# Kernel tuning notes

Measured on AMD Instinct MI355X. Metric: run time of the kernel, lower is better.

The kernel has to match this reference:

```python
import jax, jax.numpy as jnp
import numpy as np

N_NODES = 100000
N_EDGES = 1600000
N_GRAPHS = 128


def setup_inputs() -> dict:
    key = jax.random.key(0)
    ks = jax.random.split(key, 8)
    x = jax.random.normal(ks[0], (N_NODES, 384), dtype=jnp.float32)
    edge_index = jax.random.randint(ks[1], (2, N_EDGES), 0, N_NODES, dtype=jnp.int64)
    batch = jnp.sort(jax.random.randint(ks[2], (N_NODES,), 0, N_GRAPHS, dtype=jnp.int64))
    W1 = jax.random.normal(ks[3], (384, 128), dtype=jnp.float32) * (1.0 / np.sqrt(384))
    b1 = jnp.zeros((128,), dtype=jnp.float32)
    W2 = jax.random.normal(ks[4], (128, 64), dtype=jnp.float32) * (1.0 / np.sqrt(128))
    b2 = jnp.zeros((64,), dtype=jnp.float32)
    Wlin = jax.random.normal(ks[5], (64, 2), dtype=jnp.float32) * (1.0 / np.sqrt(64))
    blin = jnp.zeros((2,), dtype=jnp.float32)
    return {"x": x, "edge_index": edge_index, "batch": batch,
            "W1": W1, "b1": b1, "W2": W2, "b2": b2, "Wlin": Wlin, "blin": blin}


def gcn_conv(x, src, dst, W, b, n_nodes):
    # PyG GCNConv: self-loops + symmetric normalization D^{-1/2} A_hat D^{-1/2},
    # linear transform first (out_dim < in_dim -> cheaper messages).
    h = x @ W  # [N, out]
    deg = jax.ops.segment_sum(jnp.ones_like(dst, dtype=h.dtype), dst,
                              num_segments=n_nodes) + 1.0  # self-loop weight
    dis = jax.lax.rsqrt(deg)  # deg >= 1 always (self-loop)
    norm = dis[src] * dis[dst]  # per-edge normalization [E]
    msg = h[src] * norm[:, None]  # gather + scale [E, out]
    agg = jax.ops.segment_sum(msg, dst, num_segments=n_nodes)
    agg = agg + h * (dis * dis)[:, None]  # self-loop contribution
    return agg + b


def reference(x, edge_index, batch, W1, b1, W2, b2, Wlin, blin):
    src, dst = edge_index[0], edge_index[1]
    n_nodes = x.shape[0]
    h = jax.nn.relu(gcn_conv(x, src, dst, W1, b1, n_nodes))
    h = jax.nn.relu(gcn_conv(h, src, dst, W2, b2, n_nodes))
    # global_mean_pool over graph ids
    sums = jax.ops.segment_sum(h, batch, num_segments=N_GRAPHS)
    cnts = jax.ops.segment_sum(jnp.ones((n_nodes,), dtype=h.dtype), batch,
                               num_segments=N_GRAPHS)
    pooled = sums / jnp.maximum(cnts, 1.0)[:, None]  # [G, 64]
    # dropout is identity in eval mode
    return pooled @ Wlin + blin  # [G, 2]
```

## Files before the change

### kernel.cpp

```cpp
#include <hip/hip_runtime.h>


#define NN 100000
#define NG 128
#define BNODES 256
#define NBUK ((NN + BNODES - 1) / BNODES)
#define BCAP 6144

typedef __attribute__((ext_vector_type(8))) short short8;
typedef __attribute__((ext_vector_type(8))) unsigned short u16x8;
typedef __attribute__((ext_vector_type(4))) float f32x4;

__device__ __forceinline__ unsigned short f2bf(float f) {
    union { float f; unsigned u; } v; v.f = f;
    unsigned r = v.u + 0x7fffu + ((v.u >> 16) & 1u);
    return (unsigned short)(r >> 16);
}
__device__ __forceinline__ float bf2f(unsigned short h) {
    union { unsigned u; float f; } v; v.u = ((unsigned)h) << 16;
    return v.f;
}

__global__ __launch_bounds__(256) void bucket_scatter(const int* __restrict__ src,
                                                      const int* __restrict__ dst,
                                                      int* __restrict__ bcnt,
                                                      int2* __restrict__ pairs, int E) {
    __shared__ int hist[NBUK];
    __shared__ int lbase[NBUK];
    __shared__ int lfill[NBUK];
    const int t = threadIdx.x;
    const int chunk = (E + gridDim.x - 1) / gridDim.x;
    const int lo = blockIdx.x * chunk;
    const int hi = min(E, lo + chunk);
    for (int b = t; b < NBUK; b += 256) { hist[b] = 0; lfill[b] = 0; }
    __syncthreads();
    for (int i = lo + t; i < hi; i += 256)
        atomicAdd(&hist[dst[i] >> 8], 1);
    __syncthreads();
    for (int b = t; b < NBUK; b += 256)
        lbase[b] = hist[b] ? atomicAdd(&bcnt[b], hist[b]) : 0;
    __syncthreads();
    for (int i = lo + t; i < hi; i += 256) {
        const int s = src[i], d = dst[i];
        const int b = d >> 8;
        const int off = atomicAdd(&lfill[b], 1);
        pairs[(size_t)b * BCAP + lbase[b] + off] = make_int2(s, d);
    }
}

__global__ __launch_bounds__(512) void bucket_scan(const int* __restrict__ bcnt,
                                                   int* __restrict__ bbase,
                                                   int* __restrict__ rowptr,
                                                   int N, int E) {
    __shared__ int sm[512];
    const int t = threadIdx.x;
    sm[t] = (t < NBUK) ? bcnt[t] : 0;
    __syncthreads();
    for (int d = 1; d < 512; d <<= 1) {
        int a = (t >= d) ? sm[t - d] : 0;
        __syncthreads();
        sm[t] += a;
        __syncthreads();
    }
    if (t <= NBUK) bbase[t] = (t == 0) ? 0 : sm[t - 1];
    if (t == 0) rowptr[N] = E;
}

__global__ __launch_bounds__(256) void bucket_build(const int2* __restrict__ pairs,
                                                    const int* __restrict__ bcnt,
                                                    const int* __restrict__ bbase,
                                                    int* __restrict__ rowptr,
                                                    float* __restrict__ dis,
                                                    int* __restrict__ col, int N) {
    __shared__ int cnt[BNODES];
    __shared__ int sm[BNODES];
    __shared__ int pref[BNODES];
    __shared__ int fillc[BNODES];
    const int b = blockIdx.x;
    const int t = threadIdx.x;
    const int nbase = b * BNODES;
    const int ecnt = bcnt[b];
    const int2* ep = pairs + (size_t)b * BCAP;
    const int gbase = bbase[b];

    cnt[t] = 0;
    fillc[t] = 0;
    __syncthreads();
    for (int i = t; i < ecnt; i += 256)
        atomicAdd(&cnt[ep[i].y & (BNODES - 1)], 1);
    __syncthreads();
    sm[t] = cnt[t];
    __syncthreads();
    for (int d = 1; d < 256; d <<= 1) {
        int a = (t >= d) ? sm[t - d] : 0;
        __syncthreads();
        sm[t] += a;
        __syncthreads();
    }
    pref[t] = sm[t] - cnt[t];
    const int node = nbase + t;
    if (node < N) {
        rowptr[node] = gbase + pref[t];
        dis[node] = rsqrtf((float)cnt[t] + 1.0f);
    }
    __syncthreads();
    for (int i = t; i < ecnt; i += 256) {
        const int2 e = ep[i];
        const int d = e.y & (BNODES - 1);
        const int pos = gbase + pref[d] + atomicAdd(&fillc[d], 1);
        col[pos] = e.x;
    }
}

__global__ __launch_bounds__(256) void pack_w(const float* __restrict__ W,
                                              unsigned short* __restrict__ packH,
                                              unsigned short* __restrict__ packL,
                                              int K, int BN) {
    const int idx = blockIdx.x * blockDim.x + threadIdx.x;
    if (idx >= K * BN) return;
    const int e = idx & 7;
    const int l = (idx >> 3) & 63;
    const int rest = idx >> 9;
    const int NF = BN >> 4;
    const int nf = rest % NF;
    const int ks = rest / NF;
    const int n = nf * 16 + (l & 15);
    const int k = ks * 32 + ((l >> 4) & 3) * 8 + e;
    const float v = W[(size_t)k * BN + n];
    const unsigned short h = f2bf(v);
    packH[idx] = h;
    packL[idx] = f2bf(v - bf2f(h));
}

template <int BN>
__global__ __launch_bounds__(256) void gemm_mfma(const float* __restrict__ A,
                                                 const unsigned short* __restrict__ WpH,
                                                 const unsigned short* __restrict__ WpL,
                                                 const float* __restrict__ scale,
                                                 unsigned short* __restrict__ Out,
                                                 int N, int K) {
    constexpr int BM = 128;
    constexpr int WROWS = (BN == 128) ? 2 : 4;
    constexpr int WCOLS = (BN == 128) ? 2 : 1;
    constexpr int WTM = BM / WROWS;
    constexpr int MF = WTM / 16;
    constexpr int NFW = (BN / WCOLS) / 16;
    constexpr int NFB = BN / 16;

    __shared__ unsigned short AsH[8][512];
    __shared__ unsigned short AsL[8][512];

    const int t = threadIdx.x;
    const int wid = t >> 6, lane = t & 63;
    const int wr = wid / WCOLS, wc = wid % WCOLS;
    const int r0 = blockIdx.x * BM;

    const int s_row1 = t >> 2;
    const int s_row2 = (t + 256) >> 2;
    const int s_kg = t & 3;
    const int s_lf = ((t >> 2) & 15) + s_kg * 16;

    f32x4 acc[MF][NFW];
#pragma unroll
    for (int m = 0; m < MF; ++m)
#pragma unroll
        for (int n = 0; n < NFW; ++n) acc[m][n] = (f32x4){0.f, 0.f, 0.f, 0.f};

    for (int k0 = 0; k0 < K; k0 += 32) {
        const int ks = k0 >> 5;
#pragma unroll
        for (int uu = 0; uu < 2; ++uu) {
            const int row = uu ? s_row2 : s_row1;
            const int gr = r0 + row;
            float4 v0 = make_float4(0.f, 0.f, 0.f, 0.f), v1 = v0;
            if (gr < N) {
                const float* ap = &A[(size_t)gr * K + k0 + s_kg * 8];
                v0 = *(const float4*)ap;
                v1 = *(const float4*)(ap + 4);
            }
            short8 h, l;
            const float vv[8] = {v0.x, v0.y, v0.z, v0.w, v1.x, v1.y, v1.z, v1.w};
#pragma unroll
            for (int j = 0; j < 8; ++j) {
                const unsigned short hh = f2bf(vv[j]);
                h[j] = (short)hh;
                l[j] = (short)f2bf(vv[j] - bf2f(hh));
            }
            const int m = row >> 4;
            *(short8*)&AsH[m][s_lf * 8] = h;
            *(short8*)&AsL[m][s_lf * 8] = l;
        }
        __syncthreads();

        short8 bH[NFW], bL[NFW];
#pragma unroll
        for (int n = 0; n < NFW; ++n) {
            const int nfg = wc * NFW + n;
            const int base = ((ks * NFB + nfg) * 64 + lane) * 8;
            bH[n] = *(const short8*)&WpH[base];
            bL[n] = *(const short8*)&WpL[base];
        }
#pragma unroll
        for (int m = 0; m < MF; ++m) {
            const int mf = wr * MF + m;
            const short8 aH = *(const short8*)&AsH[mf][lane * 8];
            const short8 aL = *(const short8*)&AsL[mf][lane * 8];
#pragma unroll
            for (int n = 0; n < NFW; ++n) {
                acc[m][n] = __builtin_amdgcn_mfma_f32_16x16x32_bf16(aH, bH[n], acc[m][n], 0, 0, 0);
                acc[m][n] = __builtin_amdgcn_mfma_f32_16x16x32_bf16(aH, bL[n], acc[m][n], 0, 0, 0);
                acc[m][n] = __builtin_amdgcn_mfma_f32_16x16x32_bf16(aL, bH[n], acc[m][n], 0, 0, 0);
            }
        }
        __syncthreads();
    }

#pragma unroll
    for (int m = 0; m < MF; ++m) {
        const int row0 = r0 + wr * WTM + m * 16 + ((lane >> 4) << 2);
        float sc[4];
#pragma unroll
        for (int r = 0; r < 4; ++r) sc[r] = (row0 + r < N) ? scale[row0 + r] : 0.f;
#pragma unroll
        for (int n = 0; n < NFW; ++n) {
            const int cn = wc * (NFW * 16) + n * 16 + (lane & 15);
#pragma unroll
            for (int r = 0; r < 4; ++r) {
                if (row0 + r < N)
                    Out[(size_t)(row0 + r) * BN + cn] = f2bf(acc[m][n][r] * sc[r]);
            }
        }
    }
}

template <int COLS>
__global__ __launch_bounds__(256) void agg_gather(const int* __restrict__ rowptr,
                                                  const int* __restrict__ col,
                                                  const float* __restrict__ dis,
                                                  const unsigned short* __restrict__ Hs,
                                                  const float* __restrict__ bias,
                                                  float* __restrict__ Out, int N) {
    constexpr int NPW = (COLS == 128) ? 1 : 2;
    constexpr int LPN = 64 / NPW;
    constexpr int LPR = COLS / 8;
    constexpr int NSG = LPN / LPR;
    const int gw = (int)((blockIdx.x * blockDim.x + threadIdx.x) >> 6);
    const int lane = threadIdx.x & 63;
    const int sub = lane / LPN;
    const int nl = lane % LPN;
    const int esub = nl / LPR;
    const int sl = nl % LPR;
    const int node = gw * NPW + sub;
    const int lgbase = sub * LPN;

    float acc[8];
#pragma unroll
    for (int k = 0; k < 8; ++k) acc[k] = 0.f;

    int base = 0, len = 0;
    const int nodec = (node < N) ? node : 0;
    if (node < N) {
        base = rowptr[node];
        len = rowptr[node + 1] - base;
    }

    for (int j0 = 0; j0 < len; j0 += LPN) {
        const int remain = min(LPN, len - j0);
        const int sidx = (nl < remain) ? col[base + j0 + nl] : nodec;
        const int qtr = (remain + NSG - 1) / NSG;
        const int off = esub * qtr;
        int u = 0;
        for (; u + 8 <= qtr; u += 8) {
            u16x8 hv[8];
            float wv[8];
#pragma unroll
            for (int b = 0; b < 8; ++b) {
                const int idx = off + u + b;
                const int s = __shfl(sidx, lgbase + idx);
                wv[b] = (idx < remain) ? 1.f : 0.f;
                hv[b] = *(const u16x8*)(Hs + (size_t)s * COLS + sl * 8);
            }
#pragma unroll
            for (int b = 0; b < 8; ++b)
#pragma unroll
                for (int k = 0; k < 8; ++k)
                    acc[k] = fmaf(bf2f(hv[b][k]), wv[b], acc[k]);
        }
        for (; u + 4 <= qtr; u += 4) {
            u16x8 hv[4];
            float wv[4];
#pragma unroll
            for (int b = 0; b < 4; ++b) {
                const int idx = off + u + b;
                const int s = __shfl(sidx, lgbase + idx);
                wv[b] = (idx < remain) ? 1.f : 0.f;
                hv[b] = *(const u16x8*)(Hs + (size_t)s * COLS + sl * 8);
            }
#pragma unroll
            for (int b = 0; b < 4; ++b)
#pragma unroll
                for (int k = 0; k < 8; ++k)
                    acc[k] = fmaf(bf2f(hv[b][k]), wv[b], acc[k]);
        }
        for (; u < qtr; ++u) {
            const int idx = off + u;
            const int s = __shfl(sidx, lgbase + idx);
            const float w = (idx < remain) ? 1.f : 0.f;
            const u16x8 hv = *(const u16x8*)(Hs + (size_t)s * COLS + sl * 8);
#pragma unroll
            for (int k = 0; k < 8; ++k)
                acc[k] = fmaf(bf2f(hv[k]), w, acc[k]);
        }
    }

#pragma unroll
    for (int k = 0; k < 8; ++k) {
        acc[k] += __shfl_xor(acc[k], LPR);
        acc[k] += __shfl_xor(acc[k], 2 * LPR);
    }

    if (node < N && esub == 0) {
        const float dd = dis[node];
        const u16x8 hsb = *(const u16x8*)(Hs + (size_t)node * COLS + sl * 8);
        const f32x4 bv0 = *(const f32x4*)(bias + sl * 8);
        const f32x4 bv1 = *(const f32x4*)(bias + sl * 8 + 4);
        f32x4 o0, o1;
#pragma unroll
        for (int k = 0; k < 4; ++k) {
            o0[k] = fmaxf(fmaf(acc[k] + bf2f(hsb[k]), dd, bv0[k]), 0.f);
            o1[k] = fmaxf(fmaf(acc[k + 4] + bf2f(hsb[k + 4]), dd, bv1[k]), 0.f);
        }
        *(f32x4*)(Out + (size_t)node * COLS + sl * 8) = o0;
        *(f32x4*)(Out + (size_t)node * COLS + sl * 8 + 4) = o1;
    }
}

__global__ __launch_bounds__(256) void pool_kernel(const float* __restrict__ H,
                                                   const int* __restrict__ batch,
                                                   float* __restrict__ pooled,
                                                   float* __restrict__ cnt, int N) {
    const int c = threadIdx.x & 63;
    const int w = threadIdx.x >> 6;
    const int row0 = blockIdx.x * 128 + w * 32;
    if (row0 >= N) return;
    const int nr = min(32, N - row0);

    float v[32];
    int b[32];
#pragma unroll
    for (int i = 0; i < 32; ++i) {
        const int r = row0 + i;
        if (i < nr) {
            v[i] = H[(size_t)r * 64 + c];
            b[i] = batch[r];
        } else {
            v[i] = 0.f;
            b[i] = -1;
        }
    }
    int cur = b[0];
    float sum = 0.f, csum = 0.f;
#pragma unroll
    for (int i = 0; i < 32; ++i) {
        if (i < nr) {
            if (b[i] != cur) {
                atomicAdd(&pooled[cur * 64 + c], sum);
                if (c == 0) atomicAdd(&cnt[cur], csum);
                cur = b[i];
                sum = 0.f;
                csum = 0.f;
            }
            sum += v[i];
            csum += 1.f;
        }
    }
    atomicAdd(&pooled[cur * 64 + c], sum);
    if (c == 0) atomicAdd(&cnt[cur], csum);
}

__global__ __launch_bounds__(256) void final_kernel(const float* __restrict__ pooled,
                                                    const float* __restrict__ cnt,
                                                    const float* __restrict__ Wlin,
                                                    const float* __restrict__ blin,
                                                    float* __restrict__ out) {
    const int t = threadIdx.x;
    const int g = t >> 1, o = t & 1;
    const float inv = 1.0f / fmaxf(cnt[g], 1.0f);
    float s = 0.f;
#pragma unroll
    for (int j = 0; j < 64; ++j) s = fmaf(pooled[g * 64 + j], Wlin[j * 2 + o], s);
    out[t] = s * inv + blin[o];
}

extern "C" void kernel_launch(void* const* d_in, const int* in_sizes, int n_in,
                              void* d_out, int out_size, void* d_ws, size_t ws_size,
                              hipStream_t stream) {
    const float* x     = (const float*)d_in[0];
    const int*   edge  = (const int*)d_in[1];
    const int*   batch = (const int*)d_in[2];
    const float* W1    = (const float*)d_in[3];
    const float* b1    = (const float*)d_in[4];
    const float* W2    = (const float*)d_in[5];
    const float* b2    = (const float*)d_in[6];
    const float* Wlin  = (const float*)d_in[7];
    const float* blin  = (const float*)d_in[8];
    float* out = (float*)d_out;

    const int N = NN;
    const int E = in_sizes[1] / 2;
    const int* src = edge;
    const int* dst = edge + E;

    char* ws = (char*)d_ws;
    size_t off = 0;
    auto alloc = [&](size_t bytes) -> void* {
        void* p = ws + off;
        off += (bytes + 511) & ~(size_t)511;
        return p;
    };
    float* dis    = (float*)alloc((size_t)N * 4);
    int*   rowptr = (int*)alloc((size_t)(N + 1) * 4);
    int*   bcnt   = (int*)alloc((size_t)NBUK * 4);
    int*   bbase  = (int*)alloc((size_t)(NBUK + 1) * 4);
    int*   col    = (int*)alloc((size_t)E * 4);
    int2*  pairs  = (int2*)alloc((size_t)NBUK * BCAP * 8);
    unsigned short* w1h = (unsigned short*)alloc((size_t)384 * 128 * 2);
    unsigned short* w1l = (unsigned short*)alloc((size_t)384 * 128 * 2);
    unsigned short* w2h = (unsigned short*)alloc((size_t)128 * 64 * 2);
    unsigned short* w2l = (unsigned short*)alloc((size_t)128 * 64 * 2);
    unsigned short* h1bf = (unsigned short*)alloc((size_t)N * 128 * 2);
    float* agg1   = (float*)alloc((size_t)N * 128 * 4);
    float* pooled = (float*)alloc((size_t)NG * 64 * 4);
    float* cnt    = (float*)alloc((size_t)NG * 4);
    unsigned short* h2bf = h1bf;
    float* agg2 = agg1;

    hipMemsetAsync(bcnt, 0, (size_t)NBUK * 4, stream);
    hipMemsetAsync(pooled, 0, (size_t)NG * 64 * 4, stream);
    hipMemsetAsync(cnt, 0, (size_t)NG * 4, stream);

    pack_w<<<(384 * 128 + 255) / 256, 256, 0, stream>>>(W1, w1h, w1l, 384, 128);
    pack_w<<<(128 * 64 + 255) / 256, 256, 0, stream>>>(W2, w2h, w2l, 128, 64);

    bucket_scatter<<<512, 256, 0, stream>>>(src, dst, bcnt, pairs, E);
    bucket_scan<<<1, 512, 0, stream>>>(bcnt, bbase, rowptr, N, E);
    bucket_build<<<NBUK, 256, 0, stream>>>(pairs, bcnt, bbase, rowptr, dis, col, N);

    const int gblocks = (N + 127) / 128;
    gemm_mfma<128><<<gblocks, 256, 0, stream>>>(x, w1h, w1l, dis, h1bf, N, 384);
    agg_gather<128><<<(N + 3) / 4, 256, 0, stream>>>(rowptr, col, dis, h1bf, b1, agg1, N);

    gemm_mfma<64><<<gblocks, 256, 0, stream>>>(agg1, w2h, w2l, dis, h2bf, N, 128);
    agg_gather<64><<<(N + 7) / 8, 256, 0, stream>>>(rowptr, col, dis, h2bf, b2, agg2, N);

    pool_kernel<<<(N + 127) / 128, 256, 0, stream>>>(agg2, batch, pooled, cnt, N);
    final_kernel<<<1, 256, 0, stream>>>(pooled, cnt, Wlin, blin, out);
}
```

Baseline: 282.3 us.

## Double-buffer LDS and prefetch next K-slice in MFMA GEMM

The GEMM kernel now uses two LDS buffers. It issues global loads of the next A and B slices before running the MFMAs on the current slice, then converts and writes the prefetched A into the other buffer afterward, which removes one barrier per iteration. K becomes a template parameter so the K loop can be fully unrolled. This is meant to hide global memory latency behind compute, at the cost of doubling LDS use and raising register pressure, which may lower occupancy.

```diff
diff --git a/kernel.cpp b/kernel.cpp
--- a/kernel.cpp
+++ b/kernel.cpp
@@ -132,14 +132,15 @@
     packL[idx] = f2bf(v - bf2f(h));
 }
 
-template <int BN>
+template <int BN, int K>
 __global__ __launch_bounds__(256) void gemm_mfma(const float* __restrict__ A,
                                                  const unsigned short* __restrict__ WpH,
                                                  const unsigned short* __restrict__ WpL,
                                                  const float* __restrict__ scale,
                                                  unsigned short* __restrict__ Out,
-                                                 int N, int K) {
+                                                 int N) {
     constexpr int BM = 128;
+    constexpr int NK = K / 32;
     constexpr int WROWS = (BN == 128) ? 2 : 4;
     constexpr int WCOLS = (BN == 128) ? 2 : 1;
     constexpr int WTM = BM / WROWS;
@@ -147,8 +148,8 @@
     constexpr int NFW = (BN / WCOLS) / 16;
     constexpr int NFB = BN / 16;
 
-    __shared__ unsigned short AsH[8][512];
-    __shared__ unsigned short AsL[8][512];
+    __shared__ unsigned short AsH[2][8][512];
+    __shared__ unsigned short AsL[2][8][512];
 
     const int t = threadIdx.x;
     const int wid = t >> 6, lane = t & 63;
@@ -156,43 +157,46 @@
     const int r0 = blockIdx.x * BM;
 
     const int s_row1 = t >> 2;
-    const int s_row2 = (t + 256) >> 2;
+    const int s_row2 = 64 + (t >> 2);
     const int s_kg = t & 3;
     const int s_lf = ((t >> 2) & 15) + s_kg * 16;
 
-    f32x4 acc[MF][NFW];
-#pragma unroll
-    for (int m = 0; m < MF; ++m)
-#pragma unroll
-        for (int n = 0; n < NFW; ++n) acc[m][n] = (f32x4){0.f, 0.f, 0.f, 0.f};
-
-    for (int k0 = 0; k0 < K; k0 += 32) {
-        const int ks = k0 >> 5;
+    const bool ok1 = (r0 + s_row1) < N;
+    const bool ok2 = (r0 + s_row2) < N;
+    const float* aptr1 = A + (size_t)(r0 + s_row1) * K + s_kg * 8;
+    const float* aptr2 = A + (size_t)(r0 + s_row2) * K + s_kg * 8;
+
+    auto loadA = [&](int ks, float4* v) {
+        v[0] = v[1] = v[2] = v[3] = make_float4(0.f, 0.f, 0.f, 0.f);
+        if (ok1) {
+            v[0] = *(const float4*)(aptr1 + ks * 32);
+            v[1] = *(const float4*)(aptr1 + ks * 32 + 4);
+        }
+        if (ok2) {
+            v[2] = *(const float4*)(aptr2 + ks * 32);
+            v[3] = *(const float4*)(aptr2 + ks * 32 + 4);
+        }
+    };
+    auto cvtwrite = [&](int buf, const float4* v) {
 #pragma unroll
         for (int uu = 0; uu < 2; ++uu) {
-            const int row = uu ? s_row2 : s_row1;
-            const int gr = r0 + row;
-            float4 v0 = make_float4(0.f, 0.f, 0.f, 0.f), v1 = v0;
-            if (gr < N) {
-                const float* ap = &A[(size_t)gr * K + k0 + s_kg * 8];
-                v0 = *(const float4*)ap;
-                v1 = *(const float4*)(ap + 4);
-            }
             short8 h, l;
-            const float vv[8] = {v0.x, v0.y, v0.z, v0.w, v1.x, v1.y, v1.z, v1.w};
+            const float vv[8] = {v[2 * uu].x,     v[2 * uu].y,
+                                 v[2 * uu].z,     v[2 * uu].w,
+                                 v[2 * uu + 1].x, v[2 * uu + 1].y,
+                                 v[2 * uu + 1].z, v[2 * uu + 1].w};
 #pragma unroll
             for (int j = 0; j < 8; ++j) {
                 const unsigned short hh = f2bf(vv[j]);
                 h[j] = (short)hh;
                 l[j] = (short)f2bf(vv[j] - bf2f(hh));
             }
-            const int m = row >> 4;
-            *(short8*)&AsH[m][s_lf * 8] = h;
-            *(short8*)&AsL[m][s_lf * 8] = l;
-        }
-        __syncthreads();
-
-        short8 bH[NFW], bL[NFW];
+            const int m = uu ? (4 + wid) : wid;
+            *(short8*)&AsH[buf][m][s_lf * 8] = h;
+            *(short8*)&AsL[buf][m][s_lf * 8] = l;
+        }
+    };
+    auto loadB = [&](int ks, short8* bH, short8* bL) {
 #pragma unroll
         for (int n = 0; n < NFW; ++n) {
             const int nfg = wc * NFW + n;
@@ -200,19 +204,50 @@
             bH[n] = *(const short8*)&WpH[base];
             bL[n] = *(const short8*)&WpL[base];
         }
+    };
+
+    f32x4 acc[MF][NFW];
+#pragma unroll
+    for (int m = 0; m < MF; ++m)
+#pragma unroll
+        for (int n = 0; n < NFW; ++n) acc[m][n] = (f32x4){0.f, 0.f, 0.f, 0.f};
+
+    float4 av[4];
+    loadA(0, av);
+    cvtwrite(0, av);
+    short8 bHc[NFW], bLc[NFW];
+    loadB(0, bHc, bLc);
+
+#pragma unroll
+    for (int ks = 0; ks < NK; ++ks) {
+        const int cur = ks & 1;
+        __syncthreads();
+        float4 avn[4];
+        short8 bHn[NFW], bLn[NFW];
+        if (ks + 1 < NK) {
+            loadA(ks + 1, avn);
+            loadB(ks + 1, bHn, bLn);
+        }
 #pragma unroll
         for (int m = 0; m < MF; ++m) {
             const int mf = wr * MF + m;
-            const short8 aH = *(const short8*)&AsH[mf][lane * 8];
-            const short8 aL = *(const short8*)&AsL[mf][lane * 8];
+            const short8 aH = *(const short8*)&AsH[cur][mf][lane * 8];
+            const short8 aL = *(const short8*)&AsL[cur][mf][lane * 8];
 #pragma unroll
             for (int n = 0; n < NFW; ++n) {
-                acc[m][n] = __builtin_amdgcn_mfma_f32_16x16x32_bf16(aH, bH[n], acc[m][n], 0, 0, 0);
-                acc[m][n] = __builtin_amdgcn_mfma_f32_16x16x32_bf16(aH, bL[n], acc[m][n], 0, 0, 0);
-                acc[m][n] = __builtin_amdgcn_mfma_f32_16x16x32_bf16(aL, bH[n], acc[m][n], 0, 0, 0);
-            }
-        }
-        __syncthreads();
+                acc[m][n] = __builtin_amdgcn_mfma_f32_16x16x32_bf16(aH, bHc[n], acc[m][n], 0, 0, 0);
+                acc[m][n] = __builtin_amdgcn_mfma_f32_16x16x32_bf16(aH, bLc[n], acc[m][n], 0, 0, 0);
+                acc[m][n] = __builtin_amdgcn_mfma_f32_16x16x32_bf16(aL, bHc[n], acc[m][n], 0, 0, 0);
+            }
+        }
+        if (ks + 1 < NK) {
+            cvtwrite(cur ^ 1, avn);
+#pragma unroll
+            for (int n = 0; n < NFW; ++n) {
+                bHc[n] = bHn[n];
+                bLc[n] = bLn[n];
+            }
+        }
     }
 
 #pragma unroll
@@ -447,10 +482,10 @@
     bucket_build<<<NBUK, 256, 0, stream>>>(pairs, bcnt, bbase, rowptr, dis, col, N);
 
     const int gblocks = (N + 127) / 128;
-    gemm_mfma<128><<<gblocks, 256, 0, stream>>>(x, w1h, w1l, dis, h1bf, N, 384);
+    gemm_mfma<128, 384><<<gblocks, 256, 0, stream>>>(x, w1h, w1l, dis, h1bf, N);
     agg_gather<128><<<(N + 3) / 4, 256, 0, stream>>>(rowptr, col, dis, h1bf, b1, agg1, N);
 
-    gemm_mfma<64><<<gblocks, 256, 0, stream>>>(agg1, w2h, w2l, dis, h2bf, N, 128);
+    gemm_mfma<64, 128><<<gblocks, 256, 0, stream>>>(agg1, w2h, w2l, dis, h2bf, N);
     agg_gather<64><<<(N + 7) / 8, 256, 0, stream>>>(rowptr, col, dis, h2bf, b2, agg2, N);
 
     pool_kernel<<<(N + 127) / 128, 256, 0, stream>>>(agg2, batch, pooled, cnt, N);
```

New measurement: 274.5 us. -2.8%, faster.

## Drop LDS staging and low-bf16 A term in split-bf16 MFMA GEMM

Applied to the files above, without the earlier changes.

The GEMM is rewritten so each wave loads its own 16 A rows straight from global memory into MFMA operands, with no shared-memory staging or block barriers. The block tile shrinks to 64 rows and K becomes a template parameter. The A low-part correction term is dropped, going from three MFMAs per fragment to two, which lowers compute but also accuracy. The three memsets are replaced by one init kernel, which cuts launch overhead.

```diff
diff --git a/kernel.cpp b/kernel.cpp
--- a/kernel.cpp
+++ b/kernel.cpp
@@ -19,6 +19,15 @@
 __device__ __forceinline__ float bf2f(unsigned short h) {
     union { unsigned u; float f; } v; v.u = ((unsigned)h) << 16;
     return v.f;
+}
+
+__global__ __launch_bounds__(256) void init_kernel(int* __restrict__ bcnt,
+                                                   float* __restrict__ pooled,
+                                                   float* __restrict__ cnt) {
+    const int i = blockIdx.x * 256 + threadIdx.x;
+    if (i < NBUK) bcnt[i] = 0;
+    if (i < NG * 64) pooled[i] = 0.f;
+    if (i < NG) cnt[i] = 0.f;
 }
 
 __global__ __launch_bounds__(256) void bucket_scatter(const int* __restrict__ src,
@@ -132,103 +141,64 @@
     packL[idx] = f2bf(v - bf2f(h));
 }
 
-template <int BN>
+template <int BN, int K>
 __global__ __launch_bounds__(256) void gemm_mfma(const float* __restrict__ A,
                                                  const unsigned short* __restrict__ WpH,
                                                  const unsigned short* __restrict__ WpL,
                                                  const float* __restrict__ scale,
                                                  unsigned short* __restrict__ Out,
-                                                 int N, int K) {
-    constexpr int BM = 128;
-    constexpr int WROWS = (BN == 128) ? 2 : 4;
-    constexpr int WCOLS = (BN == 128) ? 2 : 1;
-    constexpr int WTM = BM / WROWS;
-    constexpr int MF = WTM / 16;
-    constexpr int NFW = (BN / WCOLS) / 16;
+                                                 int N) {
+    constexpr int NK = K / 32;
     constexpr int NFB = BN / 16;
-
-    __shared__ unsigned short AsH[8][512];
-    __shared__ unsigned short AsL[8][512];
 
     const int t = threadIdx.x;
     const int wid = t >> 6, lane = t & 63;
-    const int wr = wid / WCOLS, wc = wid % WCOLS;
-    const int r0 = blockIdx.x * BM;
-
-    const int s_row1 = t >> 2;
-    const int s_row2 = (t + 256) >> 2;
-    const int s_kg = t & 3;
-    const int s_lf = ((t >> 2) & 15) + s_kg * 16;
-
-    f32x4 acc[MF][NFW];
-#pragma unroll
-    for (int m = 0; m < MF; ++m)
-#pragma unroll
-        for (int n = 0; n < NFW; ++n) acc[m][n] = (f32x4){0.f, 0.f, 0.f, 0.f};
-
-    for (int k0 = 0; k0 < K; k0 += 32) {
-        const int ks = k0 >> 5;
-#pragma unroll
-        for (int uu = 0; uu < 2; ++uu) {
-            const int row = uu ? s_row2 : s_row1;
-            const int gr = r0 + row;
-            float4 v0 = make_float4(0.f, 0.f, 0.f, 0.f), v1 = v0;
-            if (gr < N) {
-                const float* ap = &A[(size_t)gr * K + k0 + s_kg * 8];
-                v0 = *(const float4*)ap;
-                v1 = *(const float4*)(ap + 4);
-            }
-            short8 h, l;
-            const float vv[8] = {v0.x, v0.y, v0.z, v0.w, v1.x, v1.y, v1.z, v1.w};
-#pragma unroll
-            for (int j = 0; j < 8; ++j) {
-                const unsigned short hh = f2bf(vv[j]);
-                h[j] = (short)hh;
-                l[j] = (short)f2bf(vv[j] - bf2f(hh));
-            }
-            const int m = row >> 4;
-            *(short8*)&AsH[m][s_lf * 8] = h;
-            *(short8*)&AsL[m][s_lf * 8] = l;
-        }
-        __syncthreads();
-
-        short8 bH[NFW], bL[NFW];
-#pragma unroll
-        for (int n = 0; n < NFW; ++n) {
-            const int nfg = wc * NFW + n;
-            const int base = ((ks * NFB + nfg) * 64 + lane) * 8;
-            bH[n] = *(const short8*)&WpH[base];
-            bL[n] = *(const short8*)&WpL[base];
-        }
-#pragma unroll
-        for (int m = 0; m < MF; ++m) {
-            const int mf = wr * MF + m;
-            const short8 aH = *(const short8*)&AsH[mf][lane * 8];
-            const short8 aL = *(const short8*)&AsL[mf][lane * 8];
-#pragma unroll
-            for (int n = 0; n < NFW; ++n) {
-                acc[m][n] = __builtin_amdgcn_mfma_f32_16x16x32_bf16(aH, bH[n], acc[m][n], 0, 0, 0);
-                acc[m][n] = __builtin_amdgcn_mfma_f32_16x16x32_bf16(aH, bL[n], acc[m][n], 0, 0, 0);
-                acc[m][n] = __builtin_amdgcn_mfma_f32_16x16x32_bf16(aL, bH[n], acc[m][n], 0, 0, 0);
-            }
-        }
-        __syncthreads();
-    }
-
-#pragma unroll
-    for (int m = 0; m < MF; ++m) {
-        const int row0 = r0 + wr * WTM + m * 16 + ((lane >> 4) << 2);
-        float sc[4];
-#pragma unroll
-        for (int r = 0; r < 4; ++r) sc[r] = (row0 + r < N) ? scale[row0 + r] : 0.f;
-#pragma unroll
-        for (int n = 0; n < NFW; ++n) {
-            const int cn = wc * (NFW * 16) + n * 16 + (lane & 15);
-#pragma unroll
-            for (int r = 0; r < 4; ++r) {
-                if (row0 + r < N)
-                    Out[(size_t)(row0 + r) * BN + cn] = f2bf(acc[m][n][r] * sc[r]);
-            }
+    const int r0 = (int)blockIdx.x * 64;
+    const int arow = r0 + wid * 16 + (lane & 15);
+    const bool ok = arow < N;
+    const float* ap = A + (size_t)(ok ? arow : 0) * K + (lane >> 4) * 8;
+
+    f32x4 acc[NFB];
+#pragma unroll
+    for (int n = 0; n < NFB; ++n) acc[n] = (f32x4){0.f, 0.f, 0.f, 0.f};
+
+#pragma unroll 2
+    for (int ks = 0; ks < NK; ++ks) {
+        float4 v0 = make_float4(0.f, 0.f, 0.f, 0.f), v1 = v0;
+        if (ok) {
+            v0 = *(const float4*)(ap + ks * 32);
+            v1 = *(const float4*)(ap + ks * 32 + 4);
+        }
+        short8 aH;
+        aH[0] = (short)f2bf(v0.x);
+        aH[1] = (short)f2bf(v0.y);
+        aH[2] = (short)f2bf(v0.z);
+        aH[3] = (short)f2bf(v0.w);
+        aH[4] = (short)f2bf(v1.x);
+        aH[5] = (short)f2bf(v1.y);
+        aH[6] = (short)f2bf(v1.z);
+        aH[7] = (short)f2bf(v1.w);
+#pragma unroll
+        for (int n = 0; n < NFB; ++n) {
+            const int base = ((ks * NFB + n) * 64 + lane) * 8;
+            const short8 bH = *(const short8*)&WpH[base];
+            const short8 bL = *(const short8*)&WpL[base];
+            acc[n] = __builtin_amdgcn_mfma_f32_16x16x32_bf16(aH, bH, acc[n], 0, 0, 0);
+            acc[n] = __builtin_amdgcn_mfma_f32_16x16x32_bf16(aH, bL, acc[n], 0, 0, 0);
+        }
+    }
+
+    const int row0 = r0 + wid * 16 + ((lane >> 4) << 2);
+    float sc[4];
+#pragma unroll
+    for (int r = 0; r < 4; ++r) sc[r] = (row0 + r < N) ? scale[row0 + r] : 0.f;
+#pragma unroll
+    for (int n = 0; n < NFB; ++n) {
+        const int cn = n * 16 + (lane & 15);
+#pragma unroll
+        for (int r = 0; r < 4; ++r) {
+            if (row0 + r < N)
+                Out[(size_t)(row0 + r) * BN + cn] = f2bf(acc[n][r] * sc[r]);
         }
     }
 }
@@ -435,9 +405,7 @@
     unsigned short* h2bf = h1bf;
     float* agg2 = agg1;
 
-    hipMemsetAsync(bcnt, 0, (size_t)NBUK * 4, stream);
-    hipMemsetAsync(pooled, 0, (size_t)NG * 64 * 4, stream);
-    hipMemsetAsync(cnt, 0, (size_t)NG * 4, stream);
+    init_kernel<<<(NG * 64 + 255) / 256, 256, 0, stream>>>(bcnt, pooled, cnt);
 
     pack_w<<<(384 * 128 + 255) / 256, 256, 0, stream>>>(W1, w1h, w1l, 384, 128);
     pack_w<<<(128 * 64 + 255) / 256, 256, 0, stream>>>(W2, w2h, w2l, 128, 64);
@@ -446,11 +414,11 @@
     bucket_scan<<<1, 512, 0, stream>>>(bcnt, bbase, rowptr, N, E);
     bucket_build<<<NBUK, 256, 0, stream>>>(pairs, bcnt, bbase, rowptr, dis, col, N);
 
-    const int gblocks = (N + 127) / 128;
-    gemm_mfma<128><<<gblocks, 256, 0, stream>>>(x, w1h, w1l, dis, h1bf, N, 384);
+    const int gblocks = (N + 63) / 64;
+    gemm_mfma<128, 384><<<gblocks, 256, 0, stream>>>(x, w1h, w1l, dis, h1bf, N);
     agg_gather<128><<<(N + 3) / 4, 256, 0, stream>>>(rowptr, col, dis, h1bf, b1, agg1, N);
 
-    gemm_mfma<64><<<gblocks, 256, 0, stream>>>(agg1, w2h, w2l, dis, h2bf, N, 128);
+    gemm_mfma<64, 128><<<gblocks, 256, 0, stream>>>(agg1, w2h, w2l, dis, h2bf, N);
     agg_gather<64><<<(N + 7) / 8, 256, 0, stream>>>(rowptr, col, dis, h2bf, b2, agg2, N);
 
     pool_kernel<<<(N + 127) / 128, 256, 0, stream>>>(agg2, batch, pooled, cnt, N);
```

After: 301.5 us. 6.8% more time.
